# Kernel optimization log

Hardware: AMD Instinct MI355X
Metric: run time of the kernel (lower is better)

The kernel has to match this reference:

```python
import jax, jax.numpy as jnp
import numpy as np

IN_DIM = 512
MEM_DIM = 512
B = 4            # branching factor
LEAVES = 16384   # perfect B-ary tree => N = (B*LEAVES - 1) // (B - 1)


def _build_tree():
    # level sizes from leaves up to root; nodes laid out level-by-level
    sizes = []
    n = LEAVES
    while n >= 1:
        sizes.append(n)
        if n == 1:
            break
        n //= B
    N = sum(sizes)
    children = -np.ones((N, B), dtype=np.int32)
    off_prev, off = 0, sizes[0]
    for l in range(1, len(sizes)):
        nl = sizes[l]
        children[off:off + nl] = off_prev + np.arange(nl * B, dtype=np.int32).reshape(nl, B)
        off_prev, off = off, off + nl
    return N, children


def setup_inputs() -> dict:
    key = jax.random.key(0)
    ks = jax.random.split(key, 9)
    N, children = _build_tree()
    sx = 1.0 / np.sqrt(IN_DIM)
    sh = 1.0 / np.sqrt(MEM_DIM)
    return {
        "x": jax.random.normal(ks[0], (N, IN_DIM), dtype=jnp.float32),
        "children": jnp.asarray(children),
        "W_ioux": jax.random.normal(ks[1], (IN_DIM, 3 * MEM_DIM), dtype=jnp.float32) * sx,
        "b_ioux": jax.random.normal(ks[2], (3 * MEM_DIM,), dtype=jnp.float32) * sx,
        "W_iouh": jax.random.normal(ks[3], (MEM_DIM, 3 * MEM_DIM), dtype=jnp.float32) * sh,
        "b_iouh": jax.random.normal(ks[4], (3 * MEM_DIM,), dtype=jnp.float32) * sh,
        "W_fx": jax.random.normal(ks[5], (IN_DIM, MEM_DIM), dtype=jnp.float32) * sx,
        "b_fx": jax.random.normal(ks[6], (MEM_DIM,), dtype=jnp.float32) * sx,
        "W_fh": jax.random.normal(ks[7], (MEM_DIM, MEM_DIM), dtype=jnp.float32) * sh,
        "b_fh": jax.random.normal(ks[8], (MEM_DIM,), dtype=jnp.float32) * sh,
    }


def _level_sizes(N, Bf):
    sizes = []
    n = (N * (Bf - 1) + 1) // Bf  # leaf count of a perfect Bf-ary tree
    while n >= 1:
        sizes.append(n)
        if n == 1:
            break
        n //= Bf
    return sizes


def reference(x, children, W_ioux, b_ioux, W_iouh, b_iouh, W_fx, b_fx, W_fh, b_fh):
    N, Bf = children.shape
    M = W_iouh.shape[0]
    sizes = _level_sizes(N, Bf)  # static Python ints

    # precompute input-side linears for ALL nodes in two big GEMMs
    x_iou = x @ W_ioux + b_ioux          # [N, 3M]
    x_f = x @ W_fx + b_fx                # [N, M]

    h_all = jnp.zeros((N, M), dtype=x.dtype)
    c_all = jnp.zeros((N, M), dtype=x.dtype)

    off = 0
    for l, nl in enumerate(sizes):
        xi = x_iou[off:off + nl]                        # [nl, 3M]
        xf = x_f[off:off + nl]                          # [nl, M]
        if l == 0:
            # leaves: single zero child (matches torch zeros(1, mem_dim))
            ch_h = jnp.zeros((nl, 1, M), dtype=x.dtype)
            ch_c = jnp.zeros((nl, 1, M), dtype=x.dtype)
        else:
            idx = children[off:off + nl]                # [nl, B]
            ch_h = h_all[idx]                           # [nl, B, M]
            ch_c = c_all[idx]
        h_sum = ch_h.sum(axis=1)                        # [nl, M]
        iou = xi + h_sum @ W_iouh + b_iouh              # [nl, 3M]
        i, o, u = jnp.split(iou, 3, axis=1)
        i = jax.nn.sigmoid(i)
        o = jax.nn.sigmoid(o)
        u = jnp.tanh(u)
        # forget gate per child: sigmoid(fh(h_k) + fx(x))
        f = jax.nn.sigmoid(jnp.einsum('nkm,mp->nkp', ch_h, W_fh) + b_fh + xf[:, None, :])
        c = i * u + (f * ch_c).sum(axis=1)              # [nl, M]
        h = o * jnp.tanh(c)
        h_all = h_all.at[off:off + nl].set(h)
        c_all = c_all.at[off:off + nl].set(c)
        off += nl

    return h_all[N - 1:N]  # root hidden state, [1, M]
```

## Files before the change

### kernel.cpp

```cpp
#include <hip/hip_runtime.h>
#include <cstdint>

using short8 = __attribute__((ext_vector_type(8))) short;
using f32x4  = __attribute__((ext_vector_type(4))) float;
typedef unsigned short ushort_t;

__device__ __forceinline__ ushort_t f2bf(float f) {
    union { float f; unsigned int u; } v; v.f = f;
    unsigned int r = v.u + 0x7FFFu + ((v.u >> 16) & 1u);
    return (ushort_t)(r >> 16);
}
__device__ __forceinline__ float bf2f(ushort_t s) {
    union { unsigned int u; float f; } v; v.u = ((unsigned int)s) << 16;
    return v.f;
}
__device__ __forceinline__ float sigmoidf(float x) { return 1.f / (1.f + expf(-x)); }

__device__ __forceinline__ void async_copy16(void* lds, const void* g) {
    __builtin_amdgcn_global_load_lds((__attribute__((address_space(1))) void*)g,
                                     (__attribute__((address_space(3))) void*)lds,
                                     16, 0, 0);
}

#define KA 1024
#define KB 1536
#define NLEAF 16384
#define NNODE 21845
#define NINT  5461

#define TAILB 512
#define NXCD  8
#define BPX   (TAILB / NXCD)

#define OFF_WTIOUX  0UL
#define OFF_WTIOUH  (OFF_WTIOUX + 1536UL*KB*2)
#define OFF_WTFX    (OFF_WTIOUH + 1536UL*KB*2)
#define OFF_WTFH    (OFF_WTFX   + 512UL*KB*2)
#define OFF_BIASIOU (OFF_WTFH   + 512UL*KB*2)
#define OFF_BIASF   (OFF_BIASIOU + 1536UL*4)
#define OFF_XHL     (OFF_BIASF  + 512UL*4)
#define OFF_HLEAF   (OFF_XHL    + 21848UL*KA*2)
#define OFF_XF      (OFF_HLEAF  + 16384UL*KA*2)
#define OFF_HSUM    (OFF_XF     + 5464UL*512*4)
#define OFF_CLEAF   (OFF_HSUM   + 4096UL*KA*2)
#define OFF_FC      (OFF_CLEAF  + 16384UL*512*4)

__global__ void wsplit_kernel(const float* __restrict__ in, ushort_t* __restrict__ out, int N) {
    __shared__ float t[32][33];
    int kb = blockIdx.x * 32, nb = blockIdx.y * 32;
    for (int i = threadIdx.y; i < 32; i += 8)
        t[i][threadIdx.x] = in[(size_t)(kb + i) * N + nb + threadIdx.x];
    __syncthreads();
    for (int i = threadIdx.y; i < 32; i += 8) {
        float v = t[threadIdx.x][i];
        ushort_t hi = f2bf(v);
        ushort_t lo = f2bf(v - bf2f(hi));
        size_t row = (size_t)(nb + i) * KB + kb + threadIdx.x;
        out[row]        = hi;
        out[row + 512]  = hi;
        out[row + 1024] = lo;
    }
}

__global__ void bias_kernel(const float* __restrict__ b_ioux, const float* __restrict__ b_iouh,
                            const float* __restrict__ b_fx, const float* __restrict__ b_fh,
                            float* __restrict__ bias_iou, float* __restrict__ bias_f,
                            unsigned* __restrict__ bar) {
    int t = blockIdx.x * blockDim.x + threadIdx.x;
    if (t < 1536) bias_iou[t] = b_ioux[t] + b_iouh[t];
    if (t < 512)  bias_f[t]   = b_fx[t] + b_fh[t];
    if (t < 160)  bar[t] = 0u;
}

__global__ void xexp_kernel(const float* __restrict__ x, ushort_t* __restrict__ xe, int n4) {
    int t = blockIdx.x * blockDim.x + threadIdx.x;
    if (t >= n4) return;
    int j = t >> 7, m4 = (t & 127) * 4;
    float4 v = *(const float4*)&x[(size_t)j * 512 + m4];
    ushort4 hi, lo;
    hi.x = f2bf(v.x); lo.x = f2bf(v.x - bf2f(hi.x));
    hi.y = f2bf(v.y); lo.y = f2bf(v.y - bf2f(hi.y));
    hi.z = f2bf(v.z); lo.z = f2bf(v.z - bf2f(hi.z));
    hi.w = f2bf(v.w); lo.w = f2bf(v.w - bf2f(hi.w));
    ushort_t* row = xe + (size_t)j * KA;
    *(ushort4*)&row[m4] = hi;
    *(ushort4*)&row[512 + m4] = lo;
}

__global__ void hsum_kernel(const ushort_t* __restrict__ h_hl, ushort_t* __restrict__ hsum_hl,
                            int n4) {
    int t = blockIdx.x * blockDim.x + threadIdx.x;
    if (t >= n4) return;
    int j = t >> 7, m4 = (t & 127) * 4;
    const ushort_t* base = h_hl + (size_t)(4 * j) * KA;
    float s0 = 0.f, s1 = 0.f, s2 = 0.f, s3 = 0.f;
#pragma unroll
    for (int r = 0; r < 4; ++r) {
        ushort4 h4 = *(const ushort4*)&base[(size_t)r * KA + m4];
        ushort4 l4 = *(const ushort4*)&base[(size_t)r * KA + 512 + m4];
        s0 += bf2f(h4.x) + bf2f(l4.x);
        s1 += bf2f(h4.y) + bf2f(l4.y);
        s2 += bf2f(h4.z) + bf2f(l4.z);
        s3 += bf2f(h4.w) + bf2f(l4.w);
    }
    ushort4 hi, lo;
    hi.x = f2bf(s0); lo.x = f2bf(s0 - bf2f(hi.x));
    hi.y = f2bf(s1); lo.y = f2bf(s1 - bf2f(hi.y));
    hi.z = f2bf(s2); lo.z = f2bf(s2 - bf2f(hi.z));
    hi.w = f2bf(s3); lo.w = f2bf(s3 - bf2f(hi.w));
    ushort_t* row = hsum_hl + (size_t)j * KA;
    *(ushort4*)&row[m4] = hi;
    *(ushort4*)&row[512 + m4] = lo;
}

__global__ __launch_bounds__(256)
void gemm_kernel(int M,
                 const ushort_t* __restrict__ a1,
                 const ushort_t* __restrict__ b1,
                 float* __restrict__ outf, int ldout) {
    __shared__ __align__(16) ushort_t Al[128 * 32];
    __shared__ __align__(16) ushort_t Bl[128 * 32];

    const int tid  = threadIdx.x;
    const int lane = tid & 63, wv = tid >> 6;
    const int l15  = lane & 15, quad = lane >> 4;
    const int wm   = wv >> 1, wn = wv & 1;
    const int m0   = blockIdx.x * 128;
    const int n0   = blockIdx.y * 128;

    const int srow = wv * 16 + (lane >> 2);
    const int kch  = ((lane & 3) ^ ((lane >> 3) & 3)) * 8;
    const int swz  = (quad ^ ((l15 >> 1) & 3)) * 8;

    const ushort_t* a1p[2]; const ushort_t* b1p[2];
#pragma unroll
    for (int r = 0; r < 2; ++r) {
        int rl = m0 + srow + r * 64; if (rl > M - 1) rl = M - 1;
        a1p[r] = a1 + (size_t)rl * KA + kch;
        int nb = n0 + srow + r * 64;
        b1p[r] = b1 + (size_t)nb * KB + kch;
    }

    f32x4 acc[4][4] = {};
    for (int k0 = 0; k0 < KB; k0 += 32) {
        int ka = (k0 < KA) ? k0 : k0 - KA;
        __syncthreads();
#pragma unroll
        for (int r = 0; r < 2; ++r) {
            async_copy16(&Al[(size_t)(wv * 16 + r * 64) * 32], a1p[r] + ka);
            async_copy16(&Bl[(size_t)(wv * 16 + r * 64) * 32], b1p[r] + k0);
        }
        __syncthreads();

        short8 aF[4], bF[4];
#pragma unroll
        for (int i = 0; i < 4; ++i) {
            aF[i] = *(const short8*)&Al[(size_t)(wm * 64 + i * 16 + l15) * 32 + swz];
            bF[i] = *(const short8*)&Bl[(size_t)(wn * 64 + i * 16 + l15) * 32 + swz];
        }
#pragma unroll
        for (int i = 0; i < 4; ++i)
#pragma unroll
            for (int j = 0; j < 4; ++j)
                acc[i][j] = __builtin_amdgcn_mfma_f32_16x16x32_bf16(aF[i], bF[j], acc[i][j], 0, 0, 0);
    }

#pragma unroll
    for (int i = 0; i < 4; ++i) {
        int mbase = m0 + wm * 64 + i * 16 + quad * 4;
#pragma unroll
        for (int j = 0; j < 4; ++j) {
            int n = n0 + wn * 64 + j * 16 + l15;
#pragma unroll
            for (int r = 0; r < 4; ++r) {
                int m = mbase + r;
                if (m < M) outf[(size_t)m * ldout + n] = acc[i][j][r];
            }
        }
    }
}

__global__ __launch_bounds__(256)
void combined_kernel(int nl,
                     const ushort_t* __restrict__ child_h, const float* __restrict__ c_prev,
                     const float* __restrict__ xf, const float* __restrict__ bias_f,
                     float* __restrict__ fc_out,
                     const ushort_t* __restrict__ x_lvl, const ushort_t* __restrict__ hsum,
                     const ushort_t* __restrict__ Wfh,
                     const ushort_t* __restrict__ Wioux, const ushort_t* __restrict__ Wiouh,
                     float* __restrict__ iou_f, ushort_t* __restrict__ iou_b) {
    __shared__ __align__(16) ushort_t Al[128 * 32];
    __shared__ __align__(16) ushort_t Bl[128 * 32];

    const int by = blockIdx.y;
    const bool fpath = by < 4;
    const int M = fpath ? 4 * nl : nl;
    const int m0 = blockIdx.x * 128;
    if (m0 >= M) return;
    const int n0 = (fpath ? by : by - 4) * 128;

    const ushort_t* A1 = fpath ? child_h : x_lvl;
    const ushort_t* A2 = fpath ? nullptr : hsum;
    const ushort_t* B1 = fpath ? Wfh : Wioux;
    const ushort_t* B2 = fpath ? nullptr : Wiouh;

    const int tid  = threadIdx.x;
    const int lane = tid & 63, wv = tid >> 6;
    const int l15  = lane & 15, quad = lane >> 4;
    const int wm   = wv >> 1, wn = wv & 1;

    const int srow = wv * 16 + (lane >> 2);
    const int kch  = ((lane & 3) ^ ((lane >> 3) & 3)) * 8;
    const int swz  = (quad ^ ((l15 >> 1) & 3)) * 8;

    const ushort_t* a1p[2]; const ushort_t* a2p[2];
    const ushort_t* b1p[2]; const ushort_t* b2p[2];
#pragma unroll
    for (int r = 0; r < 2; ++r) {
        int rl = m0 + srow + r * 64; if (rl > M - 1) rl = M - 1;
        a1p[r] = A1 + (size_t)rl * KA + kch;
        a2p[r] = A2 ? A2 + (size_t)rl * KA + kch : nullptr;
        int nb = n0 + srow + r * 64;
        b1p[r] = B1 + (size_t)nb * KB + kch;
        b2p[r] = B2 ? B2 + (size_t)nb * KB + kch : nullptr;
    }

    f32x4 acc[4][4] = {};
    const int nphase = A2 ? 2 : 1;
    for (int ph = 0; ph < nphase; ++ph) {
        for (int k0 = 0; k0 < KB; k0 += 32) {
            int ka = (k0 < KA) ? k0 : k0 - KA;
            __syncthreads();
#pragma unroll
            for (int r = 0; r < 2; ++r) {
                async_copy16(&Al[(size_t)(wv * 16 + r * 64) * 32], (ph ? a2p[r] : a1p[r]) + ka);
                async_copy16(&Bl[(size_t)(wv * 16 + r * 64) * 32], (ph ? b2p[r] : b1p[r]) + k0);
            }
            __syncthreads();

            short8 aF[4], bF[4];
#pragma unroll
            for (int i = 0; i < 4; ++i) {
                aF[i] = *(const short8*)&Al[(size_t)(wm * 64 + i * 16 + l15) * 32 + swz];
                bF[i] = *(const short8*)&Bl[(size_t)(wn * 64 + i * 16 + l15) * 32 + swz];
            }
#pragma unroll
            for (int i = 0; i < 4; ++i)
#pragma unroll
                for (int j = 0; j < 4; ++j)
                    acc[i][j] = __builtin_amdgcn_mfma_f32_16x16x32_bf16(aF[i], bF[j], acc[i][j], 0, 0, 0);
        }
    }

    if (fpath) {
#pragma unroll
        for (int i = 0; i < 4; ++i) {
            int mbase = m0 + wm * 64 + i * 16 + quad * 4;
            if (mbase < M) {
                int jg = mbase >> 2;
#pragma unroll
                for (int j = 0; j < 4; ++j) {
                    int n = n0 + wn * 64 + j * 16 + l15;
                    float add = xf[(size_t)jg * 512 + n] + bias_f[n];
                    float fc = 0.f;
#pragma unroll
                    for (int r = 0; r < 4; ++r) {
                        float f = sigmoidf(acc[i][j][r] + add);
                        fc += f * c_prev[(size_t)(mbase + r) * 512 + n];
                    }
                    fc_out[(size_t)jg * 512 + n] = fc;
                }
            }
        }
    } else {
#pragma unroll
        for (int i = 0; i < 4; ++i) {
            int mbase = m0 + wm * 64 + i * 16 + quad * 4;
#pragma unroll
            for (int j = 0; j < 4; ++j) {
                int n = n0 + wn * 64 + j * 16 + l15;
#pragma unroll
                for (int r = 0; r < 4; ++r) {
                    int m = mbase + r;
                    if (m < M) {
                        if (iou_b) iou_b[(size_t)m * 1536 + n] = f2bf(acc[i][j][r]);
                        else       iou_f[(size_t)m * 1536 + n] = acc[i][j][r];
                    }
                }
            }
        }
    }
}

__global__ __launch_bounds__(256)
void fused_leaf_kernel(int M,
                       const ushort_t* __restrict__ a1,
                       const ushort_t* __restrict__ b1,
                       const float* __restrict__ bias_iou,
                       float* __restrict__ c_out,
                       ushort_t* __restrict__ h_out) {
    __shared__ __align__(16) ushort_t Al[128 * 32];
    __shared__ __align__(16) ushort_t Bl[3 * 64 * 32];

    const int tid  = threadIdx.x;
    const int lane = tid & 63, wv = tid >> 6;
    const int l15  = lane & 15, quad = lane >> 4;
    const int m0   = blockIdx.x * 128;
    const int n0   = blockIdx.y * 64;

    const int srow = wv * 16 + (lane >> 2);
    const int kch  = ((lane & 3) ^ ((lane >> 3) & 3)) * 8;
    const int swz  = (quad ^ ((l15 >> 1) & 3)) * 8;

    const ushort_t* a1p[2]; const ushort_t* b1p[3];
#pragma unroll
    for (int r = 0; r < 2; ++r) {
        int rl = m0 + srow + r * 64; if (rl > M - 1) rl = M - 1;
        a1p[r] = a1 + (size_t)rl * KA + kch;
    }
#pragma unroll
    for (int g = 0; g < 3; ++g)
        b1p[g] = b1 + (size_t)(g * 512 + n0 + srow) * KB + kch;

    f32x4 acc[3][2][4] = {};
    for (int k0 = 0; k0 < KB; k0 += 32) {
        int ka = (k0 < KA) ? k0 : k0 - KA;
        __syncthreads();
#pragma unroll
        for (int r = 0; r < 2; ++r)
            async_copy16(&Al[(size_t)(wv * 16 + r * 64) * 32], a1p[r] + ka);
#pragma unroll
        for (int g = 0; g < 3; ++g)
            async_copy16(&Bl[(size_t)(g * 64 + wv * 16) * 32], b1p[g] + k0);
        __syncthreads();

        short8 aF[2];
#pragma unroll
        for (int i = 0; i < 2; ++i)
            aF[i] = *(const short8*)&Al[(size_t)(wv * 32 + i * 16 + l15) * 32 + swz];
#pragma unroll
        for (int g = 0; g < 3; ++g) {
            short8 bF[4];
#pragma unroll
            for (int j = 0; j < 4; ++j)
                bF[j] = *(const short8*)&Bl[(size_t)(g * 64 + j * 16 + l15) * 32 + swz];
#pragma unroll
            for (int i = 0; i < 2; ++i)
#pragma unroll
                for (int j = 0; j < 4; ++j)
                    acc[g][i][j] = __builtin_amdgcn_mfma_f32_16x16x32_bf16(aF[i], bF[j], acc[g][i][j], 0, 0, 0);
        }
    }

#pragma unroll
    for (int i = 0; i < 2; ++i) {
        int mbase = m0 + wv * 32 + i * 16 + quad * 4;
#pragma unroll
        for (int r = 0; r < 4; ++r) {
            int m = mbase + r;
            if (m < M) {
#pragma unroll
                for (int j = 0; j < 4; ++j) {
                    int n = n0 + j * 16 + l15;
                    float iv = sigmoidf(acc[0][i][j][r] + bias_iou[n]);
                    float ov = sigmoidf(acc[1][i][j][r] + bias_iou[512 + n]);
                    float uv = tanhf(  acc[2][i][j][r] + bias_iou[1024 + n]);
                    float c = iv * uv;
                    float h = ov * tanhf(c);
                    c_out[(size_t)m * 512 + n] = c;
                    ushort_t hi = f2bf(h), lo = f2bf(h - bf2f(hi));
                    h_out[(size_t)m * KA + n] = hi;
                    h_out[(size_t)m * KA + 512 + n] = lo;
                }
            }
        }
    }
}

template <bool IOU_BF>
__global__ void cell_kernel(const void* __restrict__ iou_v, const float* __restrict__ bias_iou,
                            const float* __restrict__ fc,
                            ushort_t* __restrict__ h_out, float* __restrict__ c_out,
                            int n4, float* __restrict__ outp, float* __restrict__ hf_out) {
    int t = blockIdx.x * blockDim.x + threadIdx.x;
    if (t >= n4) return;
    int j = t >> 7, m4 = (t & 127) * 4;
    float pi[4], po[4], pu[4];
    if constexpr (IOU_BF) {
        const ushort_t* row = (const ushort_t*)iou_v + (size_t)j * 1536;
        ushort4 a = *(const ushort4*)&row[m4];
        ushort4 b = *(const ushort4*)&row[512 + m4];
        ushort4 c = *(const ushort4*)&row[1024 + m4];
        pi[0]=bf2f(a.x); pi[1]=bf2f(a.y); pi[2]=bf2f(a.z); pi[3]=bf2f(a.w);
        po[0]=bf2f(b.x); po[1]=bf2f(b.y); po[2]=bf2f(b.z); po[3]=bf2f(b.w);
        pu[0]=bf2f(c.x); pu[1]=bf2f(c.y); pu[2]=bf2f(c.z); pu[3]=bf2f(c.w);
    } else {
        const float* row = (const float*)iou_v + (size_t)j * 1536;
        float4 a = *(const float4*)&row[m4];
        float4 b = *(const float4*)&row[512 + m4];
        float4 c = *(const float4*)&row[1024 + m4];
        pi[0]=a.x; pi[1]=a.y; pi[2]=a.z; pi[3]=a.w;
        po[0]=b.x; po[1]=b.y; po[2]=b.z; po[3]=b.w;
        pu[0]=c.x; pu[1]=c.y; pu[2]=c.z; pu[3]=c.w;
    }
    float4 bi = *(const float4*)&bias_iou[m4];
    float4 bo = *(const float4*)&bias_iou[512 + m4];
    float4 bu = *(const float4*)&bias_iou[1024 + m4];
    float4 fcv = *(const float4*)&fc[(size_t)j * 512 + m4];
    float bia[4] = {bi.x, bi.y, bi.z, bi.w};
    float boa[4] = {bo.x, bo.y, bo.z, bo.w};
    float bua[4] = {bu.x, bu.y, bu.z, bu.w};
    float fca[4] = {fcv.x, fcv.y, fcv.z, fcv.w};
    float cv[4], hv[4];
#pragma unroll
    for (int q = 0; q < 4; ++q) {
        float iv = sigmoidf(pi[q] + bia[q]);
        float ov = sigmoidf(po[q] + boa[q]);
        float uv = tanhf(  pu[q] + bua[q]);
        cv[q] = iv * uv + fca[q];
        hv[q] = ov * tanhf(cv[q]);
    }
    *(float4*)&c_out[(size_t)j * 512 + m4] = float4{cv[0], cv[1], cv[2], cv[3]};
    ushort4 hi, lo;
    hi.x = f2bf(hv[0]); lo.x = f2bf(hv[0] - bf2f(hi.x));
    hi.y = f2bf(hv[1]); lo.y = f2bf(hv[1] - bf2f(hi.y));
    hi.z = f2bf(hv[2]); lo.z = f2bf(hv[2] - bf2f(hi.z));
    hi.w = f2bf(hv[3]); lo.w = f2bf(hv[3] - bf2f(hi.w));
    ushort_t* hr = h_out + (size_t)j * KA;
    *(ushort4*)&hr[m4] = hi;
    *(ushort4*)&hr[512 + m4] = lo;
    if (hf_out) *(float4*)&hf_out[(size_t)j * 512 + m4] = float4{hv[0], hv[1], hv[2], hv[3]};
    if (outp) *(float4*)&outp[m4] = float4{hv[0], hv[1], hv[2], hv[3]};
}


__device__ __forceinline__ void grid_barrier(unsigned* bar, unsigned base, unsigned step) {
    __syncthreads();
    if (threadIdx.x == 0) {
        __threadfence();
        const int bkt = (int)(blockIdx.x & (NXCD - 1));
        unsigned old = __hip_atomic_fetch_add(&bar[16 * bkt], 1u, __ATOMIC_ACQ_REL, __HIP_MEMORY_SCOPE_AGENT);
        if (((old + 1u) & (unsigned)(BPX - 1)) == 0u) {
            unsigned g = __hip_atomic_fetch_add(&bar[128], 1u, __ATOMIC_ACQ_REL, __HIP_MEMORY_SCOPE_AGENT);
            if (((g + 1u) & (unsigned)(NXCD - 1)) == 0u)
                __hip_atomic_fetch_add(&bar[144], 1u, __ATOMIC_ACQ_REL, __HIP_MEMORY_SCOPE_AGENT);
        }
        while ((unsigned)(__hip_atomic_load(&bar[144], __ATOMIC_RELAXED, __HIP_MEMORY_SCOPE_AGENT) - base) < step)
            __builtin_amdgcn_s_sleep(2);
        __threadfence();
    }
    __syncthreads();
}

template <int S, int NL>
__device__ void tail_gemm(int ioff, int ioffp,
                          const float* __restrict__ x, const float* __restrict__ hf,
                          const float* __restrict__ Wx, const float* __restrict__ Wh,
                          const float* __restrict__ Wf,
                          float* __restrict__ iou_part, float* __restrict__ f_part) {
    constexpr int JG = (NL + 3) >> 2;
    int sub = (int)(blockIdx.x >> 3) * 4 + (int)(threadIdx.x >> 6);
    if (sub >= JG * S) return;
    const int n = ((int)(blockIdx.x & 7) << 6) | ((int)threadIdx.x & 63);
    const int jg = __builtin_amdgcn_readfirstlane(sub / S);
    const int s  = __builtin_amdgcn_readfirstlane(sub % S);
    const int jbase = jg << 2;

    const float* xr[4]; const float* hb[4];
#pragma unroll
    for (int p = 0; p < 4; ++p) {
        int jc = jbase + p; if (jc > NL - 1) jc = NL - 1;
        xr[p] = x + (size_t)(ioff + 16384 + jc) * 512;
        hb[p] = hf + (size_t)(ioffp - 4096 + 4 * jc) * 512;
    }
    float aI[4][3] = {}; float aF[4][4] = {};
#pragma unroll 4
    for (int k = s; k < 512; k += S) {
        const size_t kr = (size_t)k * 1536;
        float w0 = Wx[kr + n], w1 = Wx[kr + 512 + n], w2 = Wx[kr + 1024 + n];
#pragma unroll
        for (int p = 0; p < 4; ++p) {
            float xa = xr[p][k];
            aI[p][0] += xa * w0; aI[p][1] += xa * w1; aI[p][2] += xa * w2;
        }
    }
#pragma unroll 4
    for (int k = s; k < 512; k += S) {
        const size_t kr = (size_t)k * 1536;
        float w0 = Wh[kr + n], w1 = Wh[kr + 512 + n], w2 = Wh[kr + 1024 + n];
        float wf = Wf[(size_t)k * 512 + n];
#pragma unroll
        for (int p = 0; p < 4; ++p) {
            float h0 = hb[p][k], h1 = hb[p][512 + k], h2 = hb[p][1024 + k], h3 = hb[p][1536 + k];
            float hs = (h0 + h1) + (h2 + h3);
            aI[p][0] += hs * w0; aI[p][1] += hs * w1; aI[p][2] += hs * w2;
            aF[p][0] += h0 * wf; aF[p][1] += h1 * wf; aF[p][2] += h2 * wf; aF[p][3] += h3 * wf;
        }
    }
#pragma unroll
    for (int p = 0; p < 4; ++p) {
        int j = jbase + p;
        if (j < NL) {
#pragma unroll
            for (int g = 0; g < 3; ++g)
                iou_part[(((size_t)s * NL + j) * 3 + g) * 512 + n] = aI[p][g];
#pragma unroll
            for (int r = 0; r < 4; ++r)
                f_part[((size_t)s * 4 * NL + 4 * j + r) * 512 + n] = aF[p][r];
        }
    }
}

template <int S, int NL>
__device__ void tail_cell(int ioff, int ioffp,
                          float* __restrict__ hf, float* __restrict__ c_int,
                          const float* __restrict__ xf,
                          const float* __restrict__ bias_iou, const float* __restrict__ bias_f,
                          const float* __restrict__ iou_part, const float* __restrict__ f_part,
                          float* __restrict__ out) {
    int sub = (int)(blockIdx.x >> 3) * 4 + (int)(threadIdx.x >> 6);
    if (sub >= NL) return;
    const int n = ((int)(blockIdx.x & 7) << 6) | ((int)threadIdx.x & 63);
    const int j = __builtin_amdgcn_readfirstlane(sub);
    float g0 = bias_iou[n], g1 = bias_iou[512 + n], g2 = bias_iou[1024 + n];
    float f0 = 0.f, f1 = 0.f, f2 = 0.f, f3 = 0.f;
#pragma unroll 4
    for (int s = 0; s < S; ++s) {
        const float* ip = iou_part + (((size_t)s * NL + j) * 3) * 512 + n;
        g0 += ip[0]; g1 += ip[512]; g2 += ip[1024];
        const float* fp = f_part + ((size_t)s * 4 * NL + 4 * j) * 512 + n;
        f0 += fp[0]; f1 += fp[512]; f2 += fp[1024]; f3 += fp[1536];
    }
    float iv = sigmoidf(g0), ov = sigmoidf(g1), uv = tanhf(g2);
    float add = xf[(size_t)(ioff + j) * 512 + n] + bias_f[n];
    float fc = sigmoidf(f0 + add) * c_int[(size_t)(ioffp + 4 * j + 0) * 512 + n]
             + sigmoidf(f1 + add) * c_int[(size_t)(ioffp + 4 * j + 1) * 512 + n]
             + sigmoidf(f2 + add) * c_int[(size_t)(ioffp + 4 * j + 2) * 512 + n]
             + sigmoidf(f3 + add) * c_int[(size_t)(ioffp + 4 * j + 3) * 512 + n];
    float c = iv * uv + fc;
    float h = ov * tanhf(c);
    c_int[(size_t)(ioff + j) * 512 + n] = c;
    hf[(size_t)(ioff - 4096 + j) * 512 + n] = h;
    if (NL == 1) out[n] = h;
}

__global__ __launch_bounds__(256, 4)
void tail_kernel(const float* __restrict__ x, float* __restrict__ hf,
                 float* __restrict__ c_int, const float* __restrict__ xf,
                 const float* __restrict__ Wx, const float* __restrict__ Wh,
                 const float* __restrict__ Wf,
                 const float* __restrict__ bias_iou, const float* __restrict__ bias_f,
                 float* __restrict__ iou_part, float* __restrict__ f_part,
                 unsigned* __restrict__ bar, float* __restrict__ out) {
    __shared__ unsigned s_base;
    if (threadIdx.x == 0)
        s_base = __hip_atomic_load(&bar[144], __ATOMIC_RELAXED, __HIP_MEMORY_SCOPE_AGENT);
    __syncthreads();
    const unsigned base = s_base;
    unsigned step = 0;

    tail_gemm<4, 256>(5120, 4096, x, hf, Wx, Wh, Wf, iou_part, f_part);
    grid_barrier(bar, base, ++step);
    tail_cell<4, 256>(5120, 4096, hf, c_int, xf, bias_iou, bias_f, iou_part, f_part, out);
    grid_barrier(bar, base, ++step);
    tail_gemm<16, 64>(5376, 5120, x, hf, Wx, Wh, Wf, iou_part, f_part);
    grid_barrier(bar, base, ++step);
    tail_cell<16, 64>(5376, 5120, hf, c_int, xf, bias_iou, bias_f, iou_part, f_part, out);
    grid_barrier(bar, base, ++step);
    tail_gemm<64, 16>(5440, 5376, x, hf, Wx, Wh, Wf, iou_part, f_part);
    grid_barrier(bar, base, ++step);
    tail_cell<64, 16>(5440, 5376, hf, c_int, xf, bias_iou, bias_f, iou_part, f_part, out);
    grid_barrier(bar, base, ++step);
    tail_gemm<64, 4>(5456, 5440, x, hf, Wx, Wh, Wf, iou_part, f_part);
    grid_barrier(bar, base, ++step);
    tail_cell<64, 4>(5456, 5440, hf, c_int, xf, bias_iou, bias_f, iou_part, f_part, out);
    grid_barrier(bar, base, ++step);
    tail_gemm<64, 1>(5460, 5456, x, hf, Wx, Wh, Wf, iou_part, f_part);
    grid_barrier(bar, base, ++step);
    tail_cell<64, 1>(5460, 5456, hf, c_int, xf, bias_iou, bias_f, iou_part, f_part, out);
}

extern "C" void kernel_launch(void* const* d_in, const int* in_sizes, int n_in,
                              void* d_out, int out_size, void* d_ws, size_t ws_size,
                              hipStream_t stream) {
    const float* x       = (const float*)d_in[0];
    const float* W_ioux  = (const float*)d_in[2];
    const float* b_ioux  = (const float*)d_in[3];
    const float* W_iouh  = (const float*)d_in[4];
    const float* b_iouh  = (const float*)d_in[5];
    const float* W_fx    = (const float*)d_in[6];
    const float* b_fx    = (const float*)d_in[7];
    const float* W_fh    = (const float*)d_in[8];
    const float* b_fh    = (const float*)d_in[9];
    float* out = (float*)d_out;
    char* ws = (char*)d_ws;

    ushort_t* WTioux = (ushort_t*)(ws + OFF_WTIOUX);
    ushort_t* WTiouh = (ushort_t*)(ws + OFF_WTIOUH);
    ushort_t* WTfx   = (ushort_t*)(ws + OFF_WTFX);
    ushort_t* WTfh   = (ushort_t*)(ws + OFF_WTFH);
    float*    bias_iou = (float*)(ws + OFF_BIASIOU);
    float*    bias_f   = (float*)(ws + OFF_BIASF);
    ushort_t* x_hl   = (ushort_t*)(ws + OFF_XHL);
    ushort_t* h_int  = x_hl;
    ushort_t* iou_b  = x_hl + (size_t)5464 * KA;
    float*    iou_f  = (float*)iou_b;
    ushort_t* h_leaf = (ushort_t*)(ws + OFF_HLEAF);
    float*    c_int  = (float*)(ws + OFF_HLEAF);
    float*    xf32   = (float*)(ws + OFF_XF);
    ushort_t* hsum_hl= (ushort_t*)(ws + OFF_HSUM);
    float*    c_leaf = (float*)(ws + OFF_CLEAF);
    float*    fc_buf = (float*)(ws + OFF_FC);
    float*    hf32     = (float*)(ws + OFF_CLEAF);
    float*    iou_part = iou_f;
    float*    f_part   = iou_f + 1572864;
    unsigned* barp     = (unsigned*)(x_hl + (size_t)21845 * KA);

    wsplit_kernel<<<dim3(16, 48), dim3(32, 8), 0, stream>>>(W_ioux, WTioux, 1536);
    wsplit_kernel<<<dim3(16, 48), dim3(32, 8), 0, stream>>>(W_iouh, WTiouh, 1536);
    wsplit_kernel<<<dim3(16, 16), dim3(32, 8), 0, stream>>>(W_fx,   WTfx,   512);
    wsplit_kernel<<<dim3(16, 16), dim3(32, 8), 0, stream>>>(W_fh,   WTfh,   512);
    bias_kernel<<<6, 256, 0, stream>>>(b_ioux, b_iouh, b_fx, b_fh, bias_iou, bias_f, barp);

    xexp_kernel<<<(NNODE * 128 + 255) / 256, 256, 0, stream>>>(x, x_hl, NNODE * 128);

    gemm_kernel<<<dim3(43, 4), 256, 0, stream>>>(
        NINT, x_hl + (size_t)NLEAF * KA, WTfx, xf32, 512);

    fused_leaf_kernel<<<dim3(128, 8), 256, 0, stream>>>(
        NLEAF, x_hl, WTioux, bias_iou, c_leaf, h_leaf);

    {
        const int nl = 4096, n4 = nl * 128, M4 = 4 * nl;
        hsum_kernel<<<(n4 + 255) / 256, 256, 0, stream>>>(h_leaf, hsum_hl, n4);
        combined_kernel<<<dim3((M4 + 127) / 128, 16), 256, 0, stream>>>(
            nl, h_leaf, c_leaf, xf32, bias_f, fc_buf,
            x_hl + (size_t)16384 * KA, hsum_hl, WTfh, WTioux, WTiouh,
            nullptr, iou_b);
        cell_kernel<true><<<(n4 + 255) / 256, 256, 0, stream>>>(
            iou_b, bias_iou, fc_buf, h_int, c_int, n4, nullptr, nullptr);
    }
    {
        const int nl = 1024, n4 = nl * 128, M4 = 4 * nl, ioff = 4096;
        hsum_kernel<<<(n4 + 255) / 256, 256, 0, stream>>>(h_int, hsum_hl, n4);
        combined_kernel<<<dim3((M4 + 127) / 128, 16), 256, 0, stream>>>(
            nl, h_int, c_int, xf32 + (size_t)ioff * 512, bias_f, fc_buf,
            x_hl + (size_t)20480 * KA, hsum_hl, WTfh, WTioux, WTiouh,
            iou_f, nullptr);
        cell_kernel<false><<<(n4 + 255) / 256, 256, 0, stream>>>(
            iou_f, bias_iou, fc_buf, h_int + (size_t)ioff * KA, c_int + (size_t)ioff * 512,
            n4, nullptr, hf32);
    }
    tail_kernel<<<TAILB, 256, 0, stream>>>(
        x, hf32, c_int, xf32, W_ioux, W_iouh, W_fh, bias_iou, bias_f,
        iou_part, f_part, barp, out);

    (void)d_in; (void)in_sizes; (void)n_in; (void)out_size; (void)ws_size;
}
```

Baseline: 863.1 us.

## Fuse tail GEMM and cell per level with in-block LDS split-K reduction

The tail kernel used to split K across many wavefronts in different blocks, write partial sums to global memory, and run a grid barrier before a separate cell phase reduced them. Now each block's four waves split K into 128-element chunks, reduce through shared memory, and apply the LSTM cell directly. This halves the number of grid barriers and removes the global partial-sum traffic. In exchange, the deep levels with few nodes use far fewer active blocks (no cross-block K split), so those levels have less parallelism and each thread runs a longer serial K loop.

Measured after the change: 863.3 us. About the same (+0.0%).

```diff
diff --git a/kernel.cpp b/kernel.cpp
--- a/kernel.cpp
+++ b/kernel.cpp
@@ -452,19 +452,22 @@
     __syncthreads();
 }
 
-template <int S, int NL>
-__device__ void tail_gemm(int ioff, int ioffp,
-                          const float* __restrict__ x, const float* __restrict__ hf,
-                          const float* __restrict__ Wx, const float* __restrict__ Wh,
-                          const float* __restrict__ Wf,
-                          float* __restrict__ iou_part, float* __restrict__ f_part) {
+template <int NL>
+__device__ __forceinline__ void tail_level(int ioff, int ioffp,
+        const float* __restrict__ x, float* __restrict__ hf,
+        float* __restrict__ c_int, const float* __restrict__ xf,
+        const float* __restrict__ Wx, const float* __restrict__ Wh,
+        const float* __restrict__ Wf,
+        const float* __restrict__ bias_iou, const float* __restrict__ bias_f,
+        float (*red)[4][7][64], float* __restrict__ out) {
     constexpr int JG = (NL + 3) >> 2;
-    int sub = (int)(blockIdx.x >> 3) * 4 + (int)(threadIdx.x >> 6);
-    if (sub >= JG * S) return;
-    const int n = ((int)(blockIdx.x & 7) << 6) | ((int)threadIdx.x & 63);
-    const int jg = __builtin_amdgcn_readfirstlane(sub / S);
-    const int s  = __builtin_amdgcn_readfirstlane(sub % S);
+    const int jg = (int)blockIdx.x >> 3;
+    if (jg >= JG) return;
+    const int w    = (int)threadIdx.x >> 6;
+    const int lane = (int)threadIdx.x & 63;
+    const int n    = (((int)blockIdx.x & 7) << 6) | lane;
     const int jbase = jg << 2;
+    const int k0 = w << 7;
 
     const float* xr[4]; const float* hb[4];
 #pragma unroll
@@ -475,7 +478,8 @@
     }
     float aI[4][3] = {}; float aF[4][4] = {};
 #pragma unroll 4
-    for (int k = s; k < 512; k += S) {
+    for (int kk = 0; kk < 128; ++kk) {
+        const int k = k0 + kk;
         const size_t kr = (size_t)k * 1536;
         float w0 = Wx[kr + n], w1 = Wx[kr + 512 + n], w2 = Wx[kr + 1024 + n];
 #pragma unroll
@@ -485,7 +489,8 @@
         }
     }
 #pragma unroll 4
-    for (int k = s; k < 512; k += S) {
+    for (int kk = 0; kk < 128; ++kk) {
+        const int k = k0 + kk;
         const size_t kr = (size_t)k * 1536;
         float w0 = Wh[kr + n], w1 = Wh[kr + 512 + n], w2 = Wh[kr + 1024 + n];
         float wf = Wf[(size_t)k * 512 + n];
@@ -499,49 +504,36 @@
     }
 #pragma unroll
     for (int p = 0; p < 4; ++p) {
-        int j = jbase + p;
-        if (j < NL) {
-#pragma unroll
-            for (int g = 0; g < 3; ++g)
-                iou_part[(((size_t)s * NL + j) * 3 + g) * 512 + n] = aI[p][g];
-#pragma unroll
-            for (int r = 0; r < 4; ++r)
-                f_part[((size_t)s * 4 * NL + 4 * j + r) * 512 + n] = aF[p][r];
-        }
-    }
-}
-
-template <int S, int NL>
-__device__ void tail_cell(int ioff, int ioffp,
-                          float* __restrict__ hf, float* __restrict__ c_int,
-                          const float* __restrict__ xf,
-                          const float* __restrict__ bias_iou, const float* __restrict__ bias_f,
-                          const float* __restrict__ iou_part, const float* __restrict__ f_part,
-                          float* __restrict__ out) {
-    int sub = (int)(blockIdx.x >> 3) * 4 + (int)(threadIdx.x >> 6);
-    if (sub >= NL) return;
-    const int n = ((int)(blockIdx.x & 7) << 6) | ((int)threadIdx.x & 63);
-    const int j = __builtin_amdgcn_readfirstlane(sub);
-    float g0 = bias_iou[n], g1 = bias_iou[512 + n], g2 = bias_iou[1024 + n];
-    float f0 = 0.f, f1 = 0.f, f2 = 0.f, f3 = 0.f;
-#pragma unroll 4
-    for (int s = 0; s < S; ++s) {
-        const float* ip = iou_part + (((size_t)s * NL + j) * 3) * 512 + n;
-        g0 += ip[0]; g1 += ip[512]; g2 += ip[1024];
-        const float* fp = f_part + ((size_t)s * 4 * NL + 4 * j) * 512 + n;
-        f0 += fp[0]; f1 += fp[512]; f2 += fp[1024]; f3 += fp[1536];
-    }
-    float iv = sigmoidf(g0), ov = sigmoidf(g1), uv = tanhf(g2);
-    float add = xf[(size_t)(ioff + j) * 512 + n] + bias_f[n];
-    float fc = sigmoidf(f0 + add) * c_int[(size_t)(ioffp + 4 * j + 0) * 512 + n]
-             + sigmoidf(f1 + add) * c_int[(size_t)(ioffp + 4 * j + 1) * 512 + n]
-             + sigmoidf(f2 + add) * c_int[(size_t)(ioffp + 4 * j + 2) * 512 + n]
-             + sigmoidf(f3 + add) * c_int[(size_t)(ioffp + 4 * j + 3) * 512 + n];
-    float c = iv * uv + fc;
-    float h = ov * tanhf(c);
-    c_int[(size_t)(ioff + j) * 512 + n] = c;
-    hf[(size_t)(ioff - 4096 + j) * 512 + n] = h;
-    if (NL == 1) out[n] = h;
+        red[w][p][0][lane] = aI[p][0];
+        red[w][p][1][lane] = aI[p][1];
+        red[w][p][2][lane] = aI[p][2];
+        red[w][p][3][lane] = aF[p][0];
+        red[w][p][4][lane] = aF[p][1];
+        red[w][p][5][lane] = aF[p][2];
+        red[w][p][6][lane] = aF[p][3];
+    }
+    __syncthreads();
+    const int j = jbase + w;
+    if (j < NL) {
+        float v[7];
+#pragma unroll
+        for (int t = 0; t < 7; ++t)
+            v[t] = (red[0][w][t][lane] + red[1][w][t][lane])
+                 + (red[2][w][t][lane] + red[3][w][t][lane]);
+        float iv = sigmoidf(v[0] + bias_iou[n]);
+        float ov = sigmoidf(v[1] + bias_iou[512 + n]);
+        float uv = tanhf(  v[2] + bias_iou[1024 + n]);
+        float add = xf[(size_t)(ioff + j) * 512 + n] + bias_f[n];
+        float fc = sigmoidf(v[3] + add) * c_int[(size_t)(ioffp + 4 * j + 0) * 512 + n]
+                 + sigmoidf(v[4] + add) * c_int[(size_t)(ioffp + 4 * j + 1) * 512 + n]
+                 + sigmoidf(v[5] + add) * c_int[(size_t)(ioffp + 4 * j + 2) * 512 + n]
+                 + sigmoidf(v[6] + add) * c_int[(size_t)(ioffp + 4 * j + 3) * 512 + n];
+        float c = iv * uv + fc;
+        float h = ov * tanhf(c);
+        c_int[(size_t)(ioff + j) * 512 + n] = c;
+        hf[(size_t)(ioff - 4096 + j) * 512 + n] = h;
+        if (NL == 1) out[n] = h;
+    }
 }
 
 __global__ __launch_bounds__(256, 4)
@@ -550,8 +542,8 @@
                  const float* __restrict__ Wx, const float* __restrict__ Wh,
                  const float* __restrict__ Wf,
                  const float* __restrict__ bias_iou, const float* __restrict__ bias_f,
-                 float* __restrict__ iou_part, float* __restrict__ f_part,
                  unsigned* __restrict__ bar, float* __restrict__ out) {
+    __shared__ float red[4][4][7][64];
     __shared__ unsigned s_base;
     if (threadIdx.x == 0)
         s_base = __hip_atomic_load(&bar[144], __ATOMIC_RELAXED, __HIP_MEMORY_SCOPE_AGENT);
@@ -559,25 +551,15 @@
     const unsigned base = s_base;
     unsigned step = 0;
 
-    tail_gemm<4, 256>(5120, 4096, x, hf, Wx, Wh, Wf, iou_part, f_part);
+    tail_level<256>(5120, 4096, x, hf, c_int, xf, Wx, Wh, Wf, bias_iou, bias_f, red, out);
     grid_barrier(bar, base, ++step);
-    tail_cell<4, 256>(5120, 4096, hf, c_int, xf, bias_iou, bias_f, iou_part, f_part, out);
+    tail_level<64>(5376, 5120, x, hf, c_int, xf, Wx, Wh, Wf, bias_iou, bias_f, red, out);
     grid_barrier(bar, base, ++step);
-    tail_gemm<16, 64>(5376, 5120, x, hf, Wx, Wh, Wf, iou_part, f_part);
+    tail_level<16>(5440, 5376, x, hf, c_int, xf, Wx, Wh, Wf, bias_iou, bias_f, red, out);
     grid_barrier(bar, base, ++step);
-    tail_cell<16, 64>(5376, 5120, hf, c_int, xf, bias_iou, bias_f, iou_part, f_part, out);
+    tail_level<4>(5456, 5440, x, hf, c_int, xf, Wx, Wh, Wf, bias_iou, bias_f, red, out);
     grid_barrier(bar, base, ++step);
-    tail_gemm<64, 16>(5440, 5376, x, hf, Wx, Wh, Wf, iou_part, f_part);
-    grid_barrier(bar, base, ++step);
-    tail_cell<64, 16>(5440, 5376, hf, c_int, xf, bias_iou, bias_f, iou_part, f_part, out);
-    grid_barrier(bar, base, ++step);
-    tail_gemm<64, 4>(5456, 5440, x, hf, Wx, Wh, Wf, iou_part, f_part);
-    grid_barrier(bar, base, ++step);
-    tail_cell<64, 4>(5456, 5440, hf, c_int, xf, bias_iou, bias_f, iou_part, f_part, out);
-    grid_barrier(bar, base, ++step);
-    tail_gemm<64, 1>(5460, 5456, x, hf, Wx, Wh, Wf, iou_part, f_part);
-    grid_barrier(bar, base, ++step);
-    tail_cell<64, 1>(5460, 5456, hf, c_int, xf, bias_iou, bias_f, iou_part, f_part, out);
+    tail_level<1>(5460, 5456, x, hf, c_int, xf, Wx, Wh, Wf, bias_iou, bias_f, red, out);
 }
 
 extern "C" void kernel_launch(void* const* d_in, const int* in_sizes, int n_in,
@@ -612,8 +594,6 @@
     float*    c_leaf = (float*)(ws + OFF_CLEAF);
     float*    fc_buf = (float*)(ws + OFF_FC);
     float*    hf32     = (float*)(ws + OFF_CLEAF);
-    float*    iou_part = iou_f;
-    float*    f_part   = iou_f + 1572864;
     unsigned* barp     = (unsigned*)(x_hl + (size_t)21845 * KA);
 
     wsplit_kernel<<<dim3(16, 48), dim3(32, 8), 0, stream>>>(W_ioux, WTioux, 1536);
@@ -653,7 +633,7 @@
     }
     tail_kernel<<<TAILB, 256, 0, stream>>>(
         x, hf32, c_int, xf32, W_ioux, W_iouh, W_fh, bias_iou, bias_f,
-        iou_part, f_part, barp, out);
+        barp, out);
 
     (void)d_in; (void)in_sizes; (void)n_in; (void)out_size; (void)ws_size;
 }
```
